# Kernel tuning notes

Measured on AMD Instinct MI355X. Metric: run time of the kernel, lower is better.

## Reference

```python
import jax, jax.numpy as jnp
from jax import lax
import numpy as np

jax.config.update("jax_enable_x64", True)  # torch runs the Bessel recurrence in float64

D = 128            # contrast_dim / feature_num (p)
C = 1000           # num_classes
N = 256            # batch size
TEMP = 1.0         # temperature
NU = D // 2 - 1    # Bessel order nu = p/2 - 1 = 63


def log_ive_pair(x):
    """Vectorized, log-space Miller backward recurrence.

    Returns (log ive_NU(x), log ive_{NU+1}(x)) for x > 0 (float64).
    Equivalent to miller_recurrence(NU, x) in the torch source: it computes the
    ratios B_nu/B_0 and B_{nu+1}/B_0 of the backward recurrence
        B_{i-1} = (2 i / x) B_i + B_{i+1},  B_{2nu}=1, B_{2nu+1}=0,
    entirely in log space (so no isinf rescaling branches are needed), then
    anchors with i0e: log ive_nu = log i0e(x) + log B_nu - log B_0.
    """
    two_over_x = 2.0 / x
    z = jnp.zeros_like(x)

    def step(carry, i):
        s, r, a, b = carry           # s = log B_i, r = B_{i+1}/B_i
        t = two_over_x * i + r       # B_{i-1}/B_i
        s = s + jnp.log(t)           # log B_{i-1}
        a = jnp.where(i == NU + 1, s, a)  # capture log B_NU
        b = jnp.where(i == NU + 2, s, b)  # capture log B_{NU+1}
        return (s, 1.0 / t, a, b), None

    ii = jnp.arange(2 * NU, 0, -1, dtype=x.dtype)
    (s0, _, a, b), _ = lax.scan(step, (z, z, z, z), ii)  # s0 = log B_0
    li0e = jnp.log(jax.scipy.special.i0e(x))
    return li0e + a - s0, li0e + b - s0


def setup_inputs() -> dict:
    key = jax.random.key(0)
    k1, k2, k3, k4 = jax.random.split(key, 4)
    features = jax.random.normal(k1, (N, D), dtype=jnp.float32)
    features = features / jnp.linalg.norm(features, axis=1, keepdims=True)  # unit-norm embeddings
    labels = jax.random.randint(k2, (N,), 0, C, dtype=jnp.int64)
    Ave = jax.random.normal(k3, (C, D), dtype=jnp.float32)
    Ave = Ave / jnp.linalg.norm(Ave, axis=1, keepdims=True) * 0.9  # as in EstimatorCV init
    kappa = jax.random.uniform(k4, (C,), dtype=jnp.float32, minval=100.0, maxval=2000.0)
    # logc = log ive_nu(kappa) + kappa - (p/2-1) log kappa  (EstimatorCV.update_kappa)
    lnu, _ = log_ive_pair(kappa.astype(jnp.float64))
    logc = (lnu.astype(jnp.float32) + kappa - (D / 2 - 1) * jnp.log(kappa + 1e-20))
    return {"features": features, "labels": labels, "Ave": Ave, "kappa": kappa, "logc": logc}


def reference(features, labels, Ave, kappa, logc):
    # Deterministic core of ProCoUNLoss.forward (estimator updates are detached
    # state mutation; uncertainty-based resampling is a random permutation).
    Ave_norm = Ave / jnp.clip(jnp.linalg.norm(Ave, axis=1, keepdims=True), 1e-12, None)
    proto = kappa[:, None] * Ave_norm                      # [C, D]
    tem = proto[None, :, :] + features[:, None, :] / TEMP  # [N, C, D]
    kappa_new = jnp.linalg.norm(tem, axis=2)               # [N, C]
    # LogRatioC.forward: nu + k - (p/2-1) log(k+1e-20) - logc
    lnu, _ = log_ive_pair(kappa_new.astype(jnp.float64))
    contrast_logits = (lnu.astype(jnp.float32) + kappa_new
                       - (D / 2 - 1) * jnp.log(kappa_new + 1e-20)
                       - logc[None, :])                    # [N, C]
    return contrast_logits
```

## Files before the change

### kernel.cpp

```cpp
#include <hip/hip_runtime.h>
#include <hip/hip_bf16.h>
#include <math.h>

#define C_NUM 1000
#define D_NUM 128
#define N_NUM 256
#define NU    63

__device__ __constant__ double CHEB_B[25] = {
    -7.23318048787475395456E-18, -4.83050448594418207126E-18,
     4.46562142029675999901E-17,  3.46122286769746109310E-17,
    -2.82762398051658348494E-16, -3.42548561967721913462E-16,
     1.77256013305652638360E-15,  3.81168066935262242075E-15,
    -9.55484669882830764870E-15, -4.15056934728722208663E-14,
     1.54008621752140982691E-14,  3.85277838274214270114E-13,
     7.18012445138366623367E-13, -1.79417853150680611778E-12,
    -1.32158118404477131188E-11, -3.14991652796324136454E-11,
     1.18891471078464383424E-11,  4.94060238822496958910E-10,
     3.39623202570838634515E-9,   2.26666899049817806459E-8,
     2.04891858946906374183E-7,   2.89137052083475648297E-6,
     6.88975834691682398426E-5,   3.36911647825569408990E-3,
     8.04490411014108831608E-1
};

__device__ __forceinline__ double log_ive_nu(double x) {
    const double tox = 2.0 / x;
    double Bp = 0.0;
    double Bc = 1.0;
    double di = 126.0;

    #pragma unroll 7
    for (int it = 0; it < 63; ++it) {
        double Bn = fma(tox * di, Bc, Bp);
        Bp = Bc; Bc = Bn; di -= 1.0;
    }
    const double Bnu = Bc;

    #pragma unroll 7
    for (int it = 0; it < 63; ++it) {
        double Bn = fma(tox * di, Bc, Bp);
        Bp = Bc; Bc = Bn; di -= 1.0;
    }
    const double B0 = Bc;

    double y  = fma(32.0, 1.0 / x, -2.0);
    double b0 = CHEB_B[0], b1 = 0.0, b2 = 0.0;
    #pragma unroll
    for (int i = 1; i < 25; ++i) {
        b2 = b1; b1 = b0;
        b0 = y * b1 - b2 + CHEB_B[i];
    }
    double i0e = (0.5 * (b0 - b2)) / sqrt(x);

    return log(i0e * (Bnu / B0));
}

__global__ __launch_bounds__(64) void prep_proto_kernel(
        const float* __restrict__ Ave, const float* __restrict__ kappa,
        float* __restrict__ protoT) {
    const int c = blockIdx.x;
    const int t = threadIdx.x;
    float a0 = Ave[c * D_NUM + t];
    float a1 = Ave[c * D_NUM + t + 64];
    float ss = a0 * a0 + a1 * a1;
    #pragma unroll
    for (int m = 32; m; m >>= 1) ss += __shfl_xor(ss, m, 64);
    float nrm = fmaxf(sqrtf(ss), 1e-12f);
    float s   = kappa[c] / nrm;
    protoT[t * C_NUM + c]        = a0 * s;
    protoT[(t + 64) * C_NUM + c] = a1 * s;
}

#define NT 2
__global__ __launch_bounds__(256) void kappa_new_kernel(
        const float* __restrict__ features, const float* __restrict__ protoT,
        float* __restrict__ kn) {
    __shared__ float sf[NT][D_NUM];
    const int n0  = blockIdx.x * NT;
    const int tid = threadIdx.x;
    sf[tid >> 7][tid & 127] = features[n0 * D_NUM + tid];
    __syncthreads();

    float acc[NT][4] = {};
    int cc[4];
    #pragma unroll
    for (int k = 0; k < 4; ++k) cc[k] = min(tid + k * 256, C_NUM - 1);

    #pragma unroll 4
    for (int d = 0; d < D_NUM; ++d) {
        const float f0 = sf[0][d];
        const float f1 = sf[1][d];
        #pragma unroll
        for (int k = 0; k < 4; ++k) {
            float p  = protoT[d * C_NUM + cc[k]];
            float t0 = p + f0; acc[0][k] = fmaf(t0, t0, acc[0][k]);
            float t1 = p + f1; acc[1][k] = fmaf(t1, t1, acc[1][k]);
        }
    }
    #pragma unroll
    for (int k = 0; k < 4; ++k) {
        int c = tid + k * 256;
        if (c < C_NUM) {
            kn[n0 * C_NUM + c]       = sqrtf(acc[0][k]);
            kn[(n0 + 1) * C_NUM + c] = sqrtf(acc[1][k]);
        }
    }
}

__global__ __launch_bounds__(256) void logits_kernel(
        const float* __restrict__ kn, const float* __restrict__ logc,
        float* __restrict__ out) {
    const int idx = blockIdx.x * 256 + threadIdx.x;
    const int c   = idx % C_NUM;
    const float x_f = kn[idx];
    const double lnu = log_ive_nu((double)x_f);
    out[idx] = (float)lnu + x_f - 63.0f * logf(x_f + 1e-20f) - logc[c];
}

extern "C" void kernel_launch(void* const* d_in, const int* in_sizes, int n_in,
                              void* d_out, int out_size, void* d_ws, size_t ws_size,
                              hipStream_t stream) {
    const float* features = (const float*)d_in[0];
    const float* Ave   = (const float*)d_in[2];
    const float* kappa = (const float*)d_in[3];
    const float* logc  = (const float*)d_in[4];
    float* out = (float*)d_out;

    float* protoT = (float*)d_ws;
    float* kn     = (float*)((char*)d_ws + (512u << 10));

    prep_proto_kernel<<<C_NUM, 64, 0, stream>>>(Ave, kappa, protoT);
    kappa_new_kernel<<<N_NUM / NT, 256, 0, stream>>>(features, protoT, kn);
    logits_kernel<<<(N_NUM * C_NUM) / 256, 256, 0, stream>>>(kn, logc, out);
}
```

Measured before the change: 86.15 us.

## Fuse norm computation into Bessel kernel and expand norm as dot product

Merges the kappa_new and logits kernels into a single kernel, so the intermediate norms no longer travel through global memory. The squared norm is expanded algebraically as kappa^2 + |f|^2 + 2 kappa·f, with the per-class and per-sample terms precomputed in a merged prep kernel that also pads the proto stride. Each thread runs the float64 Bessel recurrence for two samples at once to expose instruction-level parallelism. The expansion can lose float32 precision through cancellation, and the fused grid has uneven class tiles (1000 classes over 4 blocks of 256) with clamped duplicate work.

Result: faster. 75.99 us (-11.8%).

```diff
diff --git a/kernel.cpp b/kernel.cpp
--- a/kernel.cpp
+++ b/kernel.cpp
@@ -6,6 +6,7 @@
 #define D_NUM 128
 #define N_NUM 256
 #define NU    63
+#define PSTRIDE 1024
 
 __device__ __constant__ double CHEB_B[25] = {
     -7.23318048787475395456E-18, -4.83050448594418207126E-18,
@@ -23,98 +24,120 @@
      8.04490411014108831608E-1
 };
 
-__device__ __forceinline__ double log_ive_nu(double x) {
-    const double tox = 2.0 / x;
-    double Bp = 0.0;
-    double Bc = 1.0;
+__device__ __forceinline__ void log_ive_nu2(double x0, double x1,
+                                            double* r0, double* r1) {
+    const double t0 = 2.0 / x0, t1 = 2.0 / x1;
+    double Bp0 = 0.0, Bc0 = 1.0;
+    double Bp1 = 0.0, Bc1 = 1.0;
     double di = 126.0;
 
-    #pragma unroll 7
+    #pragma unroll 9
     for (int it = 0; it < 63; ++it) {
-        double Bn = fma(tox * di, Bc, Bp);
-        Bp = Bc; Bc = Bn; di -= 1.0;
+        double n0 = fma(t0 * di, Bc0, Bp0);
+        double n1 = fma(t1 * di, Bc1, Bp1);
+        Bp0 = Bc0; Bc0 = n0;
+        Bp1 = Bc1; Bc1 = n1;
+        di -= 1.0;
     }
-    const double Bnu = Bc;
+    const double Bnu0 = Bc0, Bnu1 = Bc1;
 
-    #pragma unroll 7
+    #pragma unroll 9
     for (int it = 0; it < 63; ++it) {
-        double Bn = fma(tox * di, Bc, Bp);
-        Bp = Bc; Bc = Bn; di -= 1.0;
+        double n0 = fma(t0 * di, Bc0, Bp0);
+        double n1 = fma(t1 * di, Bc1, Bp1);
+        Bp0 = Bc0; Bc0 = n0;
+        Bp1 = Bc1; Bc1 = n1;
+        di -= 1.0;
     }
-    const double B0 = Bc;
 
-    double y  = fma(32.0, 1.0 / x, -2.0);
-    double b0 = CHEB_B[0], b1 = 0.0, b2 = 0.0;
+    double y0 = fma(32.0, 1.0 / x0, -2.0);
+    double y1 = fma(32.0, 1.0 / x1, -2.0);
+    double a0 = CHEB_B[0], a1 = 0.0, a2 = 0.0;
+    double c0 = CHEB_B[0], c1 = 0.0, c2 = 0.0;
     #pragma unroll
     for (int i = 1; i < 25; ++i) {
-        b2 = b1; b1 = b0;
-        b0 = y * b1 - b2 + CHEB_B[i];
+        a2 = a1; a1 = a0; a0 = y0 * a1 - a2 + CHEB_B[i];
+        c2 = c1; c1 = c0; c0 = y1 * c1 - c2 + CHEB_B[i];
     }
-    double i0e = (0.5 * (b0 - b2)) / sqrt(x);
+    double i0e0 = (0.5 * (a0 - a2)) / sqrt(x0);
+    double i0e1 = (0.5 * (c0 - c2)) / sqrt(x1);
 
-    return log(i0e * (Bnu / B0));
+    *r0 = log(i0e0 * (Bnu0 / Bc0));
+    *r1 = log(i0e1 * (Bnu1 / Bc1));
 }
 
-__global__ __launch_bounds__(64) void prep_proto_kernel(
+__global__ __launch_bounds__(256) void prep_kernel(
         const float* __restrict__ Ave, const float* __restrict__ kappa,
-        float* __restrict__ protoT) {
-    const int c = blockIdx.x;
-    const int t = threadIdx.x;
-    float a0 = Ave[c * D_NUM + t];
-    float a1 = Ave[c * D_NUM + t + 64];
-    float ss = a0 * a0 + a1 * a1;
-    #pragma unroll
-    for (int m = 32; m; m >>= 1) ss += __shfl_xor(ss, m, 64);
-    float nrm = fmaxf(sqrtf(ss), 1e-12f);
-    float s   = kappa[c] / nrm;
-    protoT[t * C_NUM + c]        = a0 * s;
-    protoT[(t + 64) * C_NUM + c] = a1 * s;
-}
-
-#define NT 2
-__global__ __launch_bounds__(256) void kappa_new_kernel(
-        const float* __restrict__ features, const float* __restrict__ protoT,
-        float* __restrict__ kn) {
-    __shared__ float sf[NT][D_NUM];
-    const int n0  = blockIdx.x * NT;
-    const int tid = threadIdx.x;
-    sf[tid >> 7][tid & 127] = features[n0 * D_NUM + tid];
-    __syncthreads();
-
-    float acc[NT][4] = {};
-    int cc[4];
-    #pragma unroll
-    for (int k = 0; k < 4; ++k) cc[k] = min(tid + k * 256, C_NUM - 1);
-
-    #pragma unroll 4
-    for (int d = 0; d < D_NUM; ++d) {
-        const float f0 = sf[0][d];
-        const float f1 = sf[1][d];
+        const float* __restrict__ features,
+        float* __restrict__ P2T, float* __restrict__ k2c, float* __restrict__ fn2) {
+    if (blockIdx.x < 250) {
+        const int w = threadIdx.x >> 6;
+        const int l = threadIdx.x & 63;
+        const int c = blockIdx.x * 4 + w;
+        float a0 = Ave[c * D_NUM + l];
+        float a1 = Ave[c * D_NUM + l + 64];
+        float ss = a0 * a0 + a1 * a1;
         #pragma unroll
-        for (int k = 0; k < 4; ++k) {
-            float p  = protoT[d * C_NUM + cc[k]];
-            float t0 = p + f0; acc[0][k] = fmaf(t0, t0, acc[0][k]);
-            float t1 = p + f1; acc[1][k] = fmaf(t1, t1, acc[1][k]);
+        for (int m = 32; m; m >>= 1) ss += __shfl_xor(ss, m, 64);
+        float nrm = fmaxf(sqrtf(ss), 1e-12f);
+        float kap = kappa[c];
+        float s2  = 2.0f * kap / nrm;
+        P2T[l * PSTRIDE + c]        = a0 * s2;
+        P2T[(l + 64) * PSTRIDE + c] = a1 * s2;
+        if (l == 0) k2c[c] = kap * kap;
+    } else {
+        const int n = threadIdx.x;
+        const float4* fr = (const float4*)(features + n * D_NUM);
+        float s = 0.0f;
+        #pragma unroll
+        for (int i = 0; i < D_NUM / 4; ++i) {
+            float4 v = fr[i];
+            s += v.x * v.x + v.y * v.y + v.z * v.z + v.w * v.w;
         }
-    }
-    #pragma unroll
-    for (int k = 0; k < 4; ++k) {
-        int c = tid + k * 256;
-        if (c < C_NUM) {
-            kn[n0 * C_NUM + c]       = sqrtf(acc[0][k]);
-            kn[(n0 + 1) * C_NUM + c] = sqrtf(acc[1][k]);
-        }
+        fn2[n] = s;
     }
 }
 
-__global__ __launch_bounds__(256) void logits_kernel(
-        const float* __restrict__ kn, const float* __restrict__ logc,
-        float* __restrict__ out) {
-    const int idx = blockIdx.x * 256 + threadIdx.x;
-    const int c   = idx % C_NUM;
-    const float x_f = kn[idx];
-    const double lnu = log_ive_nu((double)x_f);
-    out[idx] = (float)lnu + x_f - 63.0f * logf(x_f + 1e-20f) - logc[c];
+__global__ __launch_bounds__(256) void fused_kernel(
+        const float* __restrict__ P2T, const float* __restrict__ k2c,
+        const float* __restrict__ fn2, const float* __restrict__ features,
+        const float* __restrict__ logc, float* __restrict__ out) {
+    __shared__ float2 sf[D_NUM];
+    const int t  = threadIdx.x;
+    const int c  = blockIdx.x * 256 + t;
+    const int cl = min(c, C_NUM - 1);
+    const int n0 = blockIdx.y * 2;
+
+    if (t < D_NUM) {
+        sf[t] = make_float2(features[n0 * D_NUM + t],
+                            features[(n0 + 1) * D_NUM + t]);
+    }
+    __syncthreads();
+
+    float acc0 = 0.0f, acc1 = 0.0f;
+    #pragma unroll 16
+    for (int d = 0; d < D_NUM; ++d) {
+        float  p = P2T[d * PSTRIDE + cl];
+        float2 f = sf[d];
+        acc0 = fmaf(p, f.x, acc0);
+        acc1 = fmaf(p, f.y, acc1);
+    }
+
+    const float k2 = k2c[cl];
+    const float x0 = sqrtf(k2 + fn2[n0]     + acc0);
+    const float x1 = sqrtf(k2 + fn2[n0 + 1] + acc1);
+
+    double l0, l1;
+    log_ive_nu2((double)x0, (double)x1, &l0, &l1);
+
+    const float lc = logc[cl];
+    const float r0 = (float)l0 + x0 - 63.0f * logf(x0 + 1e-20f) - lc;
+    const float r1 = (float)l1 + x1 - 63.0f * logf(x1 + 1e-20f) - lc;
+
+    if (c < C_NUM) {
+        out[n0 * C_NUM + c]       = r0;
+        out[(n0 + 1) * C_NUM + c] = r1;
+    }
 }
 
 extern "C" void kernel_launch(void* const* d_in, const int* in_sizes, int n_in,
@@ -126,10 +149,10 @@
     const float* logc  = (const float*)d_in[4];
     float* out = (float*)d_out;
 
-    float* protoT = (float*)d_ws;
-    float* kn     = (float*)((char*)d_ws + (512u << 10));
+    float* P2T = (float*)d_ws;
+    float* k2c = (float*)((char*)d_ws + 524288);
+    float* fn2 = (float*)((char*)d_ws + 524288 + 4096);
 
-    prep_proto_kernel<<<C_NUM, 64, 0, stream>>>(Ave, kappa, protoT);
-    kappa_new_kernel<<<N_NUM / NT, 256, 0, stream>>>(features, protoT, kn);
-    logits_kernel<<<(N_NUM * C_NUM) / 256, 256, 0, stream>>>(kn, logc, out);
+    prep_kernel<<<251, 256, 0, stream>>>(Ave, kappa, features, P2T, k2c, fn2);
+    fused_kernel<<<dim3(4, 128), 256, 0, stream>>>(P2T, k2c, fn2, features, logc, out);
 }
```
